# Performance work log

Measured on AMD Instinct MI355X. Metric: run time of the kernel, lower is better.

## Reference

```python
import jax, jax.numpy as jnp
import numpy as np

N, K, A = 4096, 64, 8      # nodes, level-2 paths per node, attrs per l2-neighbor
D = 128                    # embed_dim
NU, NR, NA = 100000, 32, 5000  # user vocab, rating vocab, attribute vocab


def setup_inputs() -> dict:
    key = jax.random.key(0)
    ks = jax.random.split(key, 12)
    s = 0.02
    return dict(
        nodes=jax.random.randint(ks[0], (N,), 0, NU),
        paths_rel=jax.random.randint(ks[1], (N, K, 2), 0, NR),
        paths_nbr=jax.random.randint(ks[2], (N, K), 0, NU),
        attrs=jax.random.randint(ks[3], (N, K, A), 0, NA),
        u2e=jax.random.normal(ks[4], (NU, D), dtype=jnp.float32) * s,
        r2e=jax.random.normal(ks[5], (NR, D), dtype=jnp.float32) * s,
        ua2e=jax.random.normal(ks[6], (NA, D), dtype=jnp.float32) * s,
        W1=jax.random.normal(ks[7], (4 * D, 2 * D), dtype=jnp.float32) * s,
        b1=jnp.zeros((2 * D,), jnp.float32),
        W2=jax.random.normal(ks[8], (2 * D, D), dtype=jnp.float32) * s,
        b2=jnp.zeros((D,), jnp.float32),
        A1=jax.random.normal(ks[9], (2 * D, D), dtype=jnp.float32) * s,
        ab1=jnp.zeros((D,), jnp.float32),
        A2=jax.random.normal(ks[10], (D, D), dtype=jnp.float32) * s,
        ab2=jnp.zeros((D,), jnp.float32),
        A3=jax.random.normal(ks[11], (D, 1), dtype=jnp.float32) * s,
        ab3=jnp.zeros((1,), jnp.float32),
    )


def reference(nodes, paths_rel, paths_nbr, attrs, u2e, r2e, ua2e,
              W1, b1, W2, b2, A1, ab1, A2, ab2, A3, ab3):
    # per-path embedding gathers
    r1 = r2e[paths_rel[..., 0]]           # [N,K,D]
    r2 = r2e[paths_rel[..., 1]]           # [N,K,D]
    ne = u2e[paths_nbr]                   # [N,K,D]
    ae = ua2e[attrs].sum(axis=2)          # [N,K,A,D] -> [N,K,D] (uvAttrEmbedding sum)
    # concat + 2-layer MLP (w_r1, w_r2)
    x = jnp.concatenate([r1, r2, ne, ae], axis=-1)   # [N,K,4D]
    h = jax.nn.relu(x @ W1 + b1)                     # [N,K,2D]
    h = jax.nn.relu(h @ W2 + b2)                     # [N,K,D]
    # attention vs self embedding
    self_e = u2e[nodes]                              # [N,D]
    c = jnp.concatenate(
        [h, jnp.broadcast_to(self_e[:, None, :], h.shape)], axis=-1)  # [N,K,2D]
    a = jax.nn.relu(c @ A1 + ab1)
    a = jax.nn.relu(a @ A2 + ab2)
    logits = (a @ A3 + ab3)[..., 0]                  # [N,K]
    w = jax.nn.softmax(logits, axis=1)
    # attention-weighted reduce over paths
    return jnp.einsum('nk,nkd->nd', w, h)            # [N,D]
```

## Files before the change

### kernel.cpp

```cpp
#include <hip/hip_runtime.h>
#include <hip/hip_bf16.h>

#define NN 4096
#define KK 64
#define AA 8
#define DD 128

#define R1_SIZE   16896
#define XH_STRIDE 264
#define A_STRIDE  136
#define H2_STRIDE 136

typedef __bf16 bf16x8 __attribute__((ext_vector_type(8)));
typedef __bf16 bf16x2 __attribute__((ext_vector_type(2)));
typedef float  f32x4  __attribute__((ext_vector_type(4)));

__device__ __forceinline__ short f2bf(float f) {
    unsigned u = __builtin_bit_cast(unsigned, f);
    u += 0x7FFFu + ((u >> 16) & 1u);
    return (short)(u >> 16);
}
__device__ __forceinline__ float bf2f(short s) {
    unsigned u = ((unsigned)(unsigned short)s) << 16;
    return __builtin_bit_cast(float, u);
}
__device__ __forceinline__ unsigned f2bf2(float a, float b) {
#if __has_builtin(__builtin_amdgcn_cvt_pk_bf16_f32)
    bf16x2 r = __builtin_amdgcn_cvt_pk_bf16_f32(a, b);
    return __builtin_bit_cast(unsigned, r);
#else
    return ((unsigned)(unsigned short)f2bf(a)) | (((unsigned)(unsigned short)f2bf(b)) << 16);
#endif
}
__device__ __forceinline__ void store_bf8(short* dst, float4 a, float4 b) {
    uint4 v;
    v.x = f2bf2(a.x, a.y);
    v.y = f2bf2(a.z, a.w);
    v.z = f2bf2(b.x, b.y);
    v.w = f2bf2(b.z, b.w);
    *(uint4*)dst = v;
}

__global__ void prep_all(const float* __restrict__ W1, const float* __restrict__ W2,
                         const float* __restrict__ A1, const float* __restrict__ A2,
                         const int* __restrict__ nodes, const float* __restrict__ u2e,
                         const float* __restrict__ ab1,
                         short* __restrict__ W1p, short* __restrict__ W2p,
                         short* __restrict__ A1p, short* __restrict__ A2p,
                         float* __restrict__ s1g)
{
    if (blockIdx.x < 768) {
        int t = blockIdx.x * 256 + threadIdx.x;
        const float* src; short* dst; int Ncols, ksl, idx;
        if (t < 131072)      { src = W1; dst = W1p; Ncols = 256; ksl = 4; idx = t; }
        else if (t < 163840) { src = W2; dst = W2p; Ncols = 128; ksl = 3; idx = t - 131072; }
        else if (t < 180224) { src = A1; dst = A1p; Ncols = 128; ksl = 2; idx = t - 163840; }
        else                 { src = A2; dst = A2p; Ncols = 128; ksl = 2; idx = t - 180224; }
        int j     = idx & 7;
        int lane  = (idx >> 3) & 63;
        int fi    = idx >> 9;
        int kstep = fi & ((1 << ksl) - 1);
        int ntile = fi >> ksl;
        int k  = kstep * 32 + (lane >> 4) * 8 + j;
        int nn = ntile * 16 + (lane & 15);
        dst[idx] = f2bf(src[(size_t)k * Ncols + nn]);
    } else {
        __shared__ float row[2][DD];
        const int half = threadIdx.x >> 7;
        const int c    = threadIdx.x & 127;
        const int n    = (blockIdx.x - 768) * 2 + half;
        const int node = nodes[n];
        row[half][c] = u2e[(size_t)node * DD + c];
        __syncthreads();
        float acc = ab1[c];
#pragma unroll 8
        for (int i = 0; i < DD; ++i)
            acc = fmaf(row[half][i], A1[(size_t)(DD + i) * DD + c], acc);
        s1g[(size_t)n * DD + c] = acc;
    }
}

__launch_bounds__(512, 4)
__global__ void l2agg_mfma(
    const int* __restrict__ paths_rel,
    const int* __restrict__ paths_nbr,
    const int* __restrict__ attrs,
    const float* __restrict__ u2e,
    const float* __restrict__ r2e,
    const float* __restrict__ ua2e,
    const float* __restrict__ b1,
    const float* __restrict__ b2,
    const float* __restrict__ ab2,
    const float* __restrict__ A3,
    const float* __restrict__ ab3,
    const short* __restrict__ W1p,
    const short* __restrict__ W2p,
    const short* __restrict__ A1p,
    const short* __restrict__ A2p,
    const float* __restrict__ s1g,
    float* __restrict__ out)
{
    __shared__ short reg1[R1_SIZE];
    __shared__ short h2s[KK * H2_STRIDE];
    __shared__ int idx_u[576];
    float* partials = (float*)idx_u;
    float* wts      = (float*)(idx_u + 512);

    const int n    = blockIdx.x;
    const int tid  = threadIdx.x;
    const int lane = tid & 63;
    const int wv   = tid >> 6;
    const int mr   = lane & 15;
    const int q    = lane >> 4;

    {
        const int* ab = attrs + (size_t)n * KK * AA;
        __builtin_amdgcn_global_load_lds(
            (const __attribute__((address_space(1))) void*)(ab + wv * 64 + lane),
            (__attribute__((address_space(3))) void*)(idx_u + wv * 64), 4, 0, 0);
        if (wv == 0) {
            const int* nb = paths_nbr + (size_t)n * KK;
            __builtin_amdgcn_global_load_lds(
                (const __attribute__((address_space(1))) void*)(nb + lane),
                (__attribute__((address_space(3))) void*)(idx_u + 512), 4, 0, 0);
        }
    }

#pragma unroll
    for (int pass = 0; pass < 2; ++pass) {
        const int p  = pass * 32 + (tid >> 4);
        const int t  = tid & 15;
        const int o  = t * 8;
        const int pk = n * KK + p;
        const int i0 = paths_rel[pk * 2 + 0];
        const int i1 = paths_rel[pk * 2 + 1];
        float4 r1a = *(const float4*)&r2e[(size_t)i0 * DD + o];
        float4 r1b = *(const float4*)&r2e[(size_t)i0 * DD + o + 4];
        float4 r2a = *(const float4*)&r2e[(size_t)i1 * DD + o];
        float4 r2b = *(const float4*)&r2e[(size_t)i1 * DD + o + 4];
        store_bf8(&reg1[p * XH_STRIDE + o], r1a, r1b);
        store_bf8(&reg1[p * XH_STRIDE + 128 + o], r2a, r2b);
    }
    __syncthreads();

    const short* W1b = W1p + wv * 2 * 16 * 512 + lane * 8;
    f32x4 acc1[4][2] = {};
    bf16x8 bfc[2], bfn[2];
#pragma unroll
    for (int nt = 0; nt < 2; ++nt) bfc[nt] = *(const bf16x8*)&W1b[nt * 8192];
#pragma unroll
    for (int ks = 0; ks < 8; ++ks) {
#pragma unroll
        for (int nt = 0; nt < 2; ++nt)
            bfn[nt] = *(const bf16x8*)&W1b[nt * 8192 + (ks + 1) * 512];
        bf16x8 af[4];
#pragma unroll
        for (int mt = 0; mt < 4; ++mt)
            af[mt] = *(const bf16x8*)&reg1[(mt * 16 + mr) * XH_STRIDE + ks * 32 + q * 8];
#pragma unroll
        for (int nt = 0; nt < 2; ++nt)
#pragma unroll
            for (int mt = 0; mt < 4; ++mt)
                acc1[mt][nt] = __builtin_amdgcn_mfma_f32_16x16x32_bf16(af[mt], bfc[nt], acc1[mt][nt], 0, 0, 0);
#pragma unroll
        for (int nt = 0; nt < 2; ++nt) bfc[nt] = bfn[nt];
    }
    __syncthreads();

#pragma unroll
    for (int pass = 0; pass < 2; ++pass) {
        const int p  = pass * 32 + (tid >> 4);
        const int t  = tid & 15;
        const int o  = t * 8;
        const int nb = idx_u[512 + p];
        float4 nea = *(const float4*)&u2e[(size_t)nb * DD + o];
        float4 neb = *(const float4*)&u2e[(size_t)nb * DD + o + 4];
        float4 aea = make_float4(0.f, 0.f, 0.f, 0.f);
        float4 aeb = make_float4(0.f, 0.f, 0.f, 0.f);
#pragma unroll
        for (int a = 0; a < AA; ++a) {
            const int ai = idx_u[p * AA + a];
            float4 va = *(const float4*)&ua2e[(size_t)ai * DD + o];
            float4 vb = *(const float4*)&ua2e[(size_t)ai * DD + o + 4];
            aea.x += va.x; aea.y += va.y; aea.z += va.z; aea.w += va.w;
            aeb.x += vb.x; aeb.y += vb.y; aeb.z += vb.z; aeb.w += vb.w;
        }
        store_bf8(&reg1[p * XH_STRIDE + o], nea, neb);
        store_bf8(&reg1[p * XH_STRIDE + 128 + o], aea, aeb);
    }
    __syncthreads();

#pragma unroll
    for (int ks = 8; ks < 16; ++ks) {
        if (ks < 15) {
#pragma unroll
            for (int nt = 0; nt < 2; ++nt)
                bfn[nt] = *(const bf16x8*)&W1b[nt * 8192 + (ks + 1) * 512];
        }
        bf16x8 af[4];
#pragma unroll
        for (int mt = 0; mt < 4; ++mt)
            af[mt] = *(const bf16x8*)&reg1[(mt * 16 + mr) * XH_STRIDE + (ks - 8) * 32 + q * 8];
#pragma unroll
        for (int nt = 0; nt < 2; ++nt)
#pragma unroll
            for (int mt = 0; mt < 4; ++mt)
                acc1[mt][nt] = __builtin_amdgcn_mfma_f32_16x16x32_bf16(af[mt], bfc[nt], acc1[mt][nt], 0, 0, 0);
        if (ks < 15) {
#pragma unroll
            for (int nt = 0; nt < 2; ++nt) bfc[nt] = bfn[nt];
        }
    }

    const short* W2b = W2p + wv * 8 * 512 + lane * 8;
    bf16x8 g2c = *(const bf16x8*)&W2b[0], g2n;
    __syncthreads();

#pragma unroll
    for (int nt = 0; nt < 2; ++nt) {
        const int col = (wv * 2 + nt) * 16 + mr;
        const float bb = b1[col];
#pragma unroll
        for (int mt = 0; mt < 4; ++mt)
#pragma unroll
            for (int r = 0; r < 4; r += 2) {
                unsigned pk2 = f2bf2(fmaxf(acc1[mt][nt][r] + bb, 0.f),
                                     fmaxf(acc1[mt][nt][r + 1] + bb, 0.f));
                reg1[(mt * 16 + q * 4 + r)     * XH_STRIDE + col] = (short)pk2;
                reg1[(mt * 16 + q * 4 + r + 1) * XH_STRIDE + col] = (short)(pk2 >> 16);
            }
    }
    __syncthreads();

    f32x4 acc2[4] = {};
#pragma unroll
    for (int ks = 0; ks < 8; ++ks) {
        if (ks < 7) g2n = *(const bf16x8*)&W2b[(ks + 1) * 512];
        bf16x8 af[4];
#pragma unroll
        for (int mt = 0; mt < 4; ++mt)
            af[mt] = *(const bf16x8*)&reg1[(mt * 16 + mr) * XH_STRIDE + ks * 32 + q * 8];
#pragma unroll
        for (int mt = 0; mt < 4; ++mt)
            acc2[mt] = __builtin_amdgcn_mfma_f32_16x16x32_bf16(af[mt], g2c, acc2[mt], 0, 0, 0);
        if (ks < 7) g2c = g2n;
    }

    const short* A1b = A1p + wv * 4 * 512 + lane * 8;
    bf16x8 g3f[4];
#pragma unroll
    for (int ks = 0; ks < 4; ++ks) g3f[ks] = *(const bf16x8*)&A1b[ks * 512];
    const float s1v = s1g[(size_t)n * DD + wv * 16 + mr];

    {
        const int col = wv * 16 + mr;
        const float bb = b2[col];
#pragma unroll
        for (int mt = 0; mt < 4; ++mt)
#pragma unroll
            for (int r = 0; r < 4; r += 2) {
                unsigned pk2 = f2bf2(fmaxf(acc2[mt][r] + bb, 0.f),
                                     fmaxf(acc2[mt][r + 1] + bb, 0.f));
                h2s[(mt * 16 + q * 4 + r)     * H2_STRIDE + col] = (short)pk2;
                h2s[(mt * 16 + q * 4 + r + 1) * H2_STRIDE + col] = (short)(pk2 >> 16);
            }
    }
    __syncthreads();

    {
        f32x4 acc3[4];
#pragma unroll
        for (int mt = 0; mt < 4; ++mt) {
            acc3[mt][0] = s1v; acc3[mt][1] = s1v; acc3[mt][2] = s1v; acc3[mt][3] = s1v;
        }
#pragma unroll
        for (int ks = 0; ks < 4; ++ks) {
            bf16x8 af[4];
#pragma unroll
            for (int mt = 0; mt < 4; ++mt)
                af[mt] = *(const bf16x8*)&h2s[(mt * 16 + mr) * H2_STRIDE + ks * 32 + q * 8];
#pragma unroll
            for (int mt = 0; mt < 4; ++mt)
                acc3[mt] = __builtin_amdgcn_mfma_f32_16x16x32_bf16(af[mt], g3f[ks], acc3[mt], 0, 0, 0);
        }
        const short* A2b = A2p + wv * 4 * 512 + lane * 8;
        bf16x8 g4f[4];
#pragma unroll
        for (int ks = 0; ks < 4; ++ks) g4f[ks] = *(const bf16x8*)&A2b[ks * 512];

        {
            const int col = wv * 16 + mr;
#pragma unroll
            for (int mt = 0; mt < 4; ++mt)
#pragma unroll
                for (int r = 0; r < 4; r += 2) {
                    unsigned pk2 = f2bf2(fmaxf(acc3[mt][r], 0.f),
                                         fmaxf(acc3[mt][r + 1], 0.f));
                    reg1[(mt * 16 + q * 4 + r)     * A_STRIDE + col] = (short)pk2;
                    reg1[(mt * 16 + q * 4 + r + 1) * A_STRIDE + col] = (short)(pk2 >> 16);
                }
        }
        __syncthreads();

        f32x4 acc4[4];
        {
            const float bv = ab2[wv * 16 + mr];
#pragma unroll
            for (int mt = 0; mt < 4; ++mt) {
                acc4[mt][0] = bv; acc4[mt][1] = bv; acc4[mt][2] = bv; acc4[mt][3] = bv;
            }
        }
#pragma unroll
        for (int ks = 0; ks < 4; ++ks) {
            bf16x8 af[4];
#pragma unroll
            for (int mt = 0; mt < 4; ++mt)
                af[mt] = *(const bf16x8*)&reg1[(mt * 16 + mr) * A_STRIDE + ks * 32 + q * 8];
#pragma unroll
            for (int mt = 0; mt < 4; ++mt)
                acc4[mt] = __builtin_amdgcn_mfma_f32_16x16x32_bf16(af[mt], g4f[ks], acc4[mt], 0, 0, 0);
        }
        const float av = A3[wv * 16 + mr];
        float pl[4][4];
#pragma unroll
        for (int mt = 0; mt < 4; ++mt)
#pragma unroll
            for (int r = 0; r < 4; ++r)
                pl[mt][r] = fmaxf(acc4[mt][r], 0.f) * av;
#pragma unroll
        for (int off = 1; off < 16; off <<= 1)
#pragma unroll
            for (int mt = 0; mt < 4; ++mt)
#pragma unroll
                for (int r = 0; r < 4; ++r)
                    pl[mt][r] += __shfl_xor(pl[mt][r], off, 64);
        if (mr == 0) {
#pragma unroll
            for (int mt = 0; mt < 4; ++mt)
#pragma unroll
                for (int r = 0; r < 4; ++r)
                    partials[wv * KK + mt * 16 + q * 4 + r] = pl[mt][r];
        }
    }
    __syncthreads();

    if (tid < KK) {
        float l = ab3[0];
#pragma unroll
        for (int w = 0; w < 8; ++w) l += partials[w * KK + tid];
        float m = l;
#pragma unroll
        for (int off = 32; off > 0; off >>= 1) m = fmaxf(m, __shfl_xor(m, off, 64));
        float e = expf(l - m);
        float s = e;
#pragma unroll
        for (int off = 32; off > 0; off >>= 1) s += __shfl_xor(s, off, 64);
        wts[tid] = e / s;
    }
    __syncthreads();

    if (tid < DD) {
        float acc = 0.f;
#pragma unroll 8
        for (int k = 0; k < KK; ++k)
            acc = fmaf(wts[k], bf2f(h2s[k * H2_STRIDE + tid]), acc);
        out[(size_t)n * DD + tid] = acc;
    }
}

extern "C" void kernel_launch(void* const* d_in, const int* in_sizes, int n_in,
                              void* d_out, int out_size, void* d_ws, size_t ws_size,
                              hipStream_t stream)
{
    const int*   nodes     = (const int*)d_in[0];
    const int*   paths_rel = (const int*)d_in[1];
    const int*   paths_nbr = (const int*)d_in[2];
    const int*   attrs     = (const int*)d_in[3];
    const float* u2e  = (const float*)d_in[4];
    const float* r2e  = (const float*)d_in[5];
    const float* ua2e = (const float*)d_in[6];
    const float* W1   = (const float*)d_in[7];
    const float* b1   = (const float*)d_in[8];
    const float* W2   = (const float*)d_in[9];
    const float* b2   = (const float*)d_in[10];
    const float* A1   = (const float*)d_in[11];
    const float* ab1  = (const float*)d_in[12];
    const float* A2   = (const float*)d_in[13];
    const float* ab2  = (const float*)d_in[14];
    const float* A3   = (const float*)d_in[15];
    const float* ab3  = (const float*)d_in[16];
    float* out = (float*)d_out;

    short* wsp = (short*)d_ws;
    short* W1p = wsp;
    short* W2p = wsp + 131072;
    short* A1p = wsp + 163840;
    short* A2p = wsp + 180224;
    float* s1g = (float*)((char*)d_ws + 393216);

    hipLaunchKernelGGL(prep_all, dim3(768 + 2048), dim3(256), 0, stream,
                       W1, W2, A1, A2, nodes, u2e, ab1,
                       W1p, W2p, A1p, A2p, s1g);
    hipLaunchKernelGGL(l2agg_mfma, dim3(NN), dim3(512), 0, stream,
                       paths_rel, paths_nbr, attrs, u2e, r2e, ua2e,
                       b1, b2, ab2, A3, ab3,
                       W1p, W2p, A1p, A2p, s1g, out);
}
```

Baseline: 295.1 us.

## Overlap neighbor/attribute gathers with first W1 MFMA half via double LDS buffer

The main kernel now uses two LDS buffers so the neighbor-embedding and attribute-sum gathers for the second half of the concat input are issued and written into a separate buffer while the MFMAs on the rating half run. This interleaving removes a barrier and the serialized gather-then-compute phase. The self-projection prep kernel now computes four nodes per thread to reuse A1 loads and launches fewer blocks. LDS usage rises slightly, since the h2 buffer is folded into the second buffer but that buffer is larger, which may affect occupancy.

```diff
diff --git a/kernel.cpp b/kernel.cpp
--- a/kernel.cpp
+++ b/kernel.cpp
@@ -6,10 +6,10 @@
 #define AA 8
 #define DD 128
 
-#define R1_SIZE   16896
 #define XH_STRIDE 264
 #define A_STRIDE  136
 #define H2_STRIDE 136
+#define XREG_SZ   16896
 
 typedef __bf16 bf16x8 __attribute__((ext_vector_type(8)));
 typedef __bf16 bf16x2 __attribute__((ext_vector_type(2)));
@@ -34,11 +34,14 @@
 }
 __device__ __forceinline__ void store_bf8(short* dst, float4 a, float4 b) {
     uint4 v;
-    v.x = f2bf2(a.x, a.y);
-    v.y = f2bf2(a.z, a.w);
-    v.z = f2bf2(b.x, b.y);
-    v.w = f2bf2(b.z, b.w);
+    v.x = f2bf2(a.x, a.y); v.y = f2bf2(a.z, a.w);
+    v.z = f2bf2(b.x, b.y); v.w = f2bf2(b.z, b.w);
     *(uint4*)dst = v;
+}
+__device__ __forceinline__ void store_bf4(short* dst, float4 a) {
+    uint2 v;
+    v.x = f2bf2(a.x, a.y); v.y = f2bf2(a.z, a.w);
+    *(uint2*)dst = v;
 }
 
 __global__ void prep_all(const float* __restrict__ W1, const float* __restrict__ W2,
@@ -65,18 +68,28 @@
         int nn = ntile * 16 + (lane & 15);
         dst[idx] = f2bf(src[(size_t)k * Ncols + nn]);
     } else {
-        __shared__ float row[2][DD];
-        const int half = threadIdx.x >> 7;
-        const int c    = threadIdx.x & 127;
-        const int n    = (blockIdx.x - 768) * 2 + half;
-        const int node = nodes[n];
-        row[half][c] = u2e[(size_t)node * DD + c];
+        __shared__ float rows[8][DD];
+        const int b = blockIdx.x - 768;
+        {
+            const int r  = threadIdx.x >> 5;
+            const int c4 = (threadIdx.x & 31) * 4;
+            const int node = nodes[b * 8 + r];
+            *(float4*)&rows[r][c4] = *(const float4*)&u2e[(size_t)node * DD + c4];
+        }
         __syncthreads();
-        float acc = ab1[c];
-#pragma unroll 8
-        for (int i = 0; i < DD; ++i)
-            acc = fmaf(row[half][i], A1[(size_t)(DD + i) * DD + c], acc);
-        s1g[(size_t)n * DD + c] = acc;
+        const int h = threadIdx.x >> 7;
+        const int c = threadIdx.x & 127;
+        const float ab = ab1[c];
+        float acc[4] = {ab, ab, ab, ab};
+        for (int i = 0; i < DD; ++i) {
+            const float av = A1[(size_t)(DD + i) * DD + c];
+#pragma unroll
+            for (int j = 0; j < 4; ++j)
+                acc[j] = fmaf(rows[h * 4 + j][i], av, acc[j]);
+        }
+#pragma unroll
+        for (int j = 0; j < 4; ++j)
+            s1g[(size_t)(b * 8 + h * 4 + j) * DD + c] = acc[j];
     }
 }
 
@@ -100,8 +113,8 @@
     const float* __restrict__ s1g,
     float* __restrict__ out)
 {
-    __shared__ short reg1[R1_SIZE];
-    __shared__ short h2s[KK * H2_STRIDE];
+    __shared__ short xa[XREG_SZ];
+    __shared__ short xb[XREG_SZ];
     __shared__ int idx_u[576];
     float* partials = (float*)idx_u;
     float* wts      = (float*)(idx_u + 512);
@@ -138,8 +151,8 @@
         float4 r1b = *(const float4*)&r2e[(size_t)i0 * DD + o + 4];
         float4 r2a = *(const float4*)&r2e[(size_t)i1 * DD + o];
         float4 r2b = *(const float4*)&r2e[(size_t)i1 * DD + o + 4];
-        store_bf8(&reg1[p * XH_STRIDE + o], r1a, r1b);
-        store_bf8(&reg1[p * XH_STRIDE + 128 + o], r2a, r2b);
+        store_bf8(&xa[p * XH_STRIDE + o], r1a, r1b);
+        store_bf8(&xa[p * XH_STRIDE + 128 + o], r2a, r2b);
     }
     __syncthreads();
 
@@ -148,45 +161,70 @@
     bf16x8 bfc[2], bfn[2];
 #pragma unroll
     for (int nt = 0; nt < 2; ++nt) bfc[nt] = *(const bf16x8*)&W1b[nt * 8192];
-#pragma unroll
-    for (int ks = 0; ks < 8; ++ks) {
-#pragma unroll
-        for (int nt = 0; nt < 2; ++nt)
-            bfn[nt] = *(const bf16x8*)&W1b[nt * 8192 + (ks + 1) * 512];
-        bf16x8 af[4];
-#pragma unroll
-        for (int mt = 0; mt < 4; ++mt)
-            af[mt] = *(const bf16x8*)&reg1[(mt * 16 + mr) * XH_STRIDE + ks * 32 + q * 8];
-#pragma unroll
-        for (int nt = 0; nt < 2; ++nt)
-#pragma unroll
-            for (int mt = 0; mt < 4; ++mt)
-                acc1[mt][nt] = __builtin_amdgcn_mfma_f32_16x16x32_bf16(af[mt], bfc[nt], acc1[mt][nt], 0, 0, 0);
-#pragma unroll
-        for (int nt = 0; nt < 2; ++nt) bfc[nt] = bfn[nt];
-    }
-    __syncthreads();
-
-#pragma unroll
-    for (int pass = 0; pass < 2; ++pass) {
-        const int p  = pass * 32 + (tid >> 4);
-        const int t  = tid & 15;
-        const int o  = t * 8;
+
+    const int sp = tid >> 5;
+    const int so = (tid & 31) * 4;
+
+#pragma unroll
+    for (int step = 0; step < 4; ++step) {
+        const int p  = step * 16 + sp;
         const int nb = idx_u[512 + p];
-        float4 nea = *(const float4*)&u2e[(size_t)nb * DD + o];
-        float4 neb = *(const float4*)&u2e[(size_t)nb * DD + o + 4];
-        float4 aea = make_float4(0.f, 0.f, 0.f, 0.f);
-        float4 aeb = make_float4(0.f, 0.f, 0.f, 0.f);
-#pragma unroll
-        for (int a = 0; a < AA; ++a) {
-            const int ai = idx_u[p * AA + a];
-            float4 va = *(const float4*)&ua2e[(size_t)ai * DD + o];
-            float4 vb = *(const float4*)&ua2e[(size_t)ai * DD + o + 4];
-            aea.x += va.x; aea.y += va.y; aea.z += va.z; aea.w += va.w;
-            aeb.x += vb.x; aeb.y += vb.y; aeb.z += vb.z; aeb.w += vb.w;
-        }
-        store_bf8(&reg1[p * XH_STRIDE + o], nea, neb);
-        store_bf8(&reg1[p * XH_STRIDE + 128 + o], aea, aeb);
+        const int4 ai0 = *(const int4*)&idx_u[p * 8];
+        const int4 ai1 = *(const int4*)&idx_u[p * 8 + 4];
+        float4 nev = *(const float4*)&u2e[(size_t)nb * DD + so];
+        float4 g0 = *(const float4*)&ua2e[(size_t)ai0.x * DD + so];
+        float4 g1 = *(const float4*)&ua2e[(size_t)ai0.y * DD + so];
+        float4 g2 = *(const float4*)&ua2e[(size_t)ai0.z * DD + so];
+        float4 g3 = *(const float4*)&ua2e[(size_t)ai0.w * DD + so];
+        {
+            const int ks = 2 * step;
+#pragma unroll
+            for (int nt = 0; nt < 2; ++nt)
+                bfn[nt] = *(const bf16x8*)&W1b[nt * 8192 + (ks + 1) * 512];
+            bf16x8 af[4];
+#pragma unroll
+            for (int mt = 0; mt < 4; ++mt)
+                af[mt] = *(const bf16x8*)&xa[(mt * 16 + mr) * XH_STRIDE + ks * 32 + q * 8];
+#pragma unroll
+            for (int nt = 0; nt < 2; ++nt)
+#pragma unroll
+                for (int mt = 0; mt < 4; ++mt)
+                    acc1[mt][nt] = __builtin_amdgcn_mfma_f32_16x16x32_bf16(af[mt], bfc[nt], acc1[mt][nt], 0, 0, 0);
+#pragma unroll
+            for (int nt = 0; nt < 2; ++nt) bfc[nt] = bfn[nt];
+        }
+        float4 s4;
+        s4.x = (g0.x + g1.x) + (g2.x + g3.x);
+        s4.y = (g0.y + g1.y) + (g2.y + g3.y);
+        s4.z = (g0.z + g1.z) + (g2.z + g3.z);
+        s4.w = (g0.w + g1.w) + (g2.w + g3.w);
+        store_bf4(&xb[p * XH_STRIDE + so], nev);
+        float4 g4 = *(const float4*)&ua2e[(size_t)ai1.x * DD + so];
+        float4 g5 = *(const float4*)&ua2e[(size_t)ai1.y * DD + so];
+        float4 g6 = *(const float4*)&ua2e[(size_t)ai1.z * DD + so];
+        float4 g7 = *(const float4*)&ua2e[(size_t)ai1.w * DD + so];
+        {
+            const int ks = 2 * step + 1;
+#pragma unroll
+            for (int nt = 0; nt < 2; ++nt)
+                bfn[nt] = *(const bf16x8*)&W1b[nt * 8192 + (ks + 1) * 512];
+            bf16x8 af[4];
+#pragma unroll
+            for (int mt = 0; mt < 4; ++mt)
+                af[mt] = *(const bf16x8*)&xa[(mt * 16 + mr) * XH_STRIDE + ks * 32 + q * 8];
+#pragma unroll
+            for (int nt = 0; nt < 2; ++nt)
+#pragma unroll
+                for (int mt = 0; mt < 4; ++mt)
+                    acc1[mt][nt] = __builtin_amdgcn_mfma_f32_16x16x32_bf16(af[mt], bfc[nt], acc1[mt][nt], 0, 0, 0);
+#pragma unroll
+            for (int nt = 0; nt < 2; ++nt) bfc[nt] = bfn[nt];
+        }
+        s4.x += (g4.x + g5.x) + (g6.x + g7.x);
+        s4.y += (g4.y + g5.y) + (g6.y + g7.y);
+        s4.z += (g4.z + g5.z) + (g6.z + g7.z);
+        s4.w += (g4.w + g5.w) + (g6.w + g7.w);
+        store_bf4(&xb[p * XH_STRIDE + 128 + so], s4);
     }
     __syncthreads();
 
@@ -200,7 +238,7 @@
         bf16x8 af[4];
 #pragma unroll
         for (int mt = 0; mt < 4; ++mt)
-            af[mt] = *(const bf16x8*)&reg1[(mt * 16 + mr) * XH_STRIDE + (ks - 8) * 32 + q * 8];
+            af[mt] = *(const bf16x8*)&xb[(mt * 16 + mr) * XH_STRIDE + (ks - 8) * 32 + q * 8];
 #pragma unroll
         for (int nt = 0; nt < 2; ++nt)
 #pragma unroll
@@ -214,7 +252,6 @@
 
     const short* W2b = W2p + wv * 8 * 512 + lane * 8;
     bf16x8 g2c = *(const bf16x8*)&W2b[0], g2n;
-    __syncthreads();
 
 #pragma unroll
     for (int nt = 0; nt < 2; ++nt) {
@@ -226,8 +263,8 @@
             for (int r = 0; r < 4; r += 2) {
                 unsigned pk2 = f2bf2(fmaxf(acc1[mt][nt][r] + bb, 0.f),
                                      fmaxf(acc1[mt][nt][r + 1] + bb, 0.f));
-                reg1[(mt * 16 + q * 4 + r)     * XH_STRIDE + col] = (short)pk2;
-                reg1[(mt * 16 + q * 4 + r + 1) * XH_STRIDE + col] = (short)(pk2 >> 16);
+                xa[(mt * 16 + q * 4 + r)     * XH_STRIDE + col] = (short)pk2;
+                xa[(mt * 16 + q * 4 + r + 1) * XH_STRIDE + col] = (short)(pk2 >> 16);
             }
     }
     __syncthreads();
@@ -239,7 +276,7 @@
         bf16x8 af[4];
 #pragma unroll
         for (int mt = 0; mt < 4; ++mt)
-            af[mt] = *(const bf16x8*)&reg1[(mt * 16 + mr) * XH_STRIDE + ks * 32 + q * 8];
+            af[mt] = *(const bf16x8*)&xa[(mt * 16 + mr) * XH_STRIDE + ks * 32 + q * 8];
 #pragma unroll
         for (int mt = 0; mt < 4; ++mt)
             acc2[mt] = __builtin_amdgcn_mfma_f32_16x16x32_bf16(af[mt], g2c, acc2[mt], 0, 0, 0);
@@ -261,8 +298,8 @@
             for (int r = 0; r < 4; r += 2) {
                 unsigned pk2 = f2bf2(fmaxf(acc2[mt][r] + bb, 0.f),
                                      fmaxf(acc2[mt][r + 1] + bb, 0.f));
-                h2s[(mt * 16 + q * 4 + r)     * H2_STRIDE + col] = (short)pk2;
-                h2s[(mt * 16 + q * 4 + r + 1) * H2_STRIDE + col] = (short)(pk2 >> 16);
+                xb[(mt * 16 + q * 4 + r)     * H2_STRIDE + col] = (short)pk2;
+                xb[(mt * 16 + q * 4 + r + 1) * H2_STRIDE + col] = (short)(pk2 >> 16);
             }
     }
     __syncthreads();
@@ -278,7 +315,7 @@
             bf16x8 af[4];
 #pragma unroll
             for (int mt = 0; mt < 4; ++mt)
-                af[mt] = *(const bf16x8*)&h2s[(mt * 16 + mr) * H2_STRIDE + ks * 32 + q * 8];
+                af[mt] = *(const bf16x8*)&xb[(mt * 16 + mr) * H2_STRIDE + ks * 32 + q * 8];
 #pragma unroll
             for (int mt = 0; mt < 4; ++mt)
                 acc3[mt] = __builtin_amdgcn_mfma_f32_16x16x32_bf16(af[mt], g3f[ks], acc3[mt], 0, 0, 0);
@@ -296,8 +333,8 @@
                 for (int r = 0; r < 4; r += 2) {
                     unsigned pk2 = f2bf2(fmaxf(acc3[mt][r], 0.f),
                                          fmaxf(acc3[mt][r + 1], 0.f));
-                    reg1[(mt * 16 + q * 4 + r)     * A_STRIDE + col] = (short)pk2;
-                    reg1[(mt * 16 + q * 4 + r + 1) * A_STRIDE + col] = (short)(pk2 >> 16);
+                    xa[(mt * 16 + q * 4 + r)     * A_STRIDE + col] = (short)pk2;
+                    xa[(mt * 16 + q * 4 + r + 1) * A_STRIDE + col] = (short)(pk2 >> 16);
                 }
         }
         __syncthreads();
@@ -315,7 +352,7 @@
             bf16x8 af[4];
 #pragma unroll
             for (int mt = 0; mt < 4; ++mt)
-                af[mt] = *(const bf16x8*)&reg1[(mt * 16 + mr) * A_STRIDE + ks * 32 + q * 8];
+                af[mt] = *(const bf16x8*)&xa[(mt * 16 + mr) * A_STRIDE + ks * 32 + q * 8];
 #pragma unroll
             for (int mt = 0; mt < 4; ++mt)
                 acc4[mt] = __builtin_amdgcn_mfma_f32_16x16x32_bf16(af[mt], g4f[ks], acc4[mt], 0, 0, 0);
@@ -363,7 +400,7 @@
         float acc = 0.f;
 #pragma unroll 8
         for (int k = 0; k < KK; ++k)
-            acc = fmaf(wts[k], bf2f(h2s[k * H2_STRIDE + tid]), acc);
+            acc = fmaf(wts[k], bf2f(xb[k * H2_STRIDE + tid]), acc);
         out[(size_t)n * DD + tid] = acc;
     }
 }
@@ -398,7 +435,7 @@
     short* A2p = wsp + 180224;
     float* s1g = (float*)((char*)d_ws + 393216);
 
-    hipLaunchKernelGGL(prep_all, dim3(768 + 2048), dim3(256), 0, stream,
+    hipLaunchKernelGGL(prep_all, dim3(768 + 512), dim3(256), 0, stream,
                        W1, W2, A1, A2, nodes, u2e, ab1,
                        W1p, W2p, A1p, A2p, s1g);
     hipLaunchKernelGGL(l2agg_mfma, dim3(NN), dim3(512), 0, stream,
```

Result: no change. 298.0 us (+1.0%).
